# Performance work log

Hardware: AMD Instinct MI355X
Metric: run time of the kernel (lower is better)

## Reference

```python
import jax, jax.numpy as jnp
import numpy as np

SEQ, BATCH, N_IN, N_HID, N_OUT = 2048, 64, 256, 512, 128


def setup_inputs() -> dict:
    key = jax.random.key(0)
    ks = jax.random.split(key, 7)
    s_ih = 1.0 / np.sqrt(N_IN)
    s_hh = 1.0 / np.sqrt(N_HID)
    return {
        "x": jax.random.normal(ks[0], (SEQ, BATCH, N_IN), dtype=jnp.float32),
        # PyTorch Linear stores weight as (out_features, in_features)
        "W_ih": jax.random.uniform(ks[1], (N_HID, N_IN), jnp.float32, -s_ih, s_ih),
        "b_ih": jax.random.uniform(ks[2], (N_HID,), jnp.float32, -s_ih, s_ih),
        "W_hh": jax.random.uniform(ks[3], (N_HID, N_HID), jnp.float32, -s_hh, s_hh),
        "b_hh": jax.random.uniform(ks[4], (N_HID,), jnp.float32, -s_hh, s_hh),
        "W_ho": jax.random.uniform(ks[5], (N_OUT, N_HID), jnp.float32, -s_hh, s_hh),
        "b_ho": jax.random.uniform(ks[6], (N_OUT,), jnp.float32, -s_hh, s_hh),
    }


def reference(x, W_ih, b_ih, W_hh, b_hh, W_ho, b_ho):
    # hidden init: torch.zeros(1, n_hidden) broadcasts to (batch, n_hidden)
    h0 = jnp.zeros((x.shape[1], W_hh.shape[0]), dtype=x.dtype)

    def step(h, xt):
        # new_h = tanh(Linear_ih(x_t) + Linear_hh(h))
        h_new = jnp.tanh(xt @ W_ih.T + b_ih + h @ W_hh.T + b_hh)
        return h_new, None

    h_final, _ = jax.lax.scan(step, h0, x)
    return h_final @ W_ho.T + b_ho  # (batch, n_output)
```

## Files before the change

kernel.cpp:

```cpp
#include <hip/hip_runtime.h>
#include <math.h>

#define SEQ   2048
#define BATCH 64
#define NIN   256
#define NHID  512
#define NOUT  128

#define NSL 4
#define JSL 128

#define WIRE_WORDS (2*BATCH*NSL*256)
#define WIRE_BYTES ((size_t)WIRE_WORDS*4)
#define HFIN_BYTES ((size_t)BATCH*NHID*4)
#define XP_BYTES   ((size_t)SEQ*BATCH*NHID*4)

typedef unsigned int u32;
typedef u32 u32x2 __attribute__((ext_vector_type(2)));

__device__ __forceinline__ u32x2 ld8_ic(const u32* p) {
  u32x2 r;
  asm volatile("global_load_dwordx2 %0, %1, off sc0 sc1"
               : "=v"(r) : "v"(p) : "memory");
  return r;
}
__device__ __forceinline__ void st8_ic(u32* p, u32x2 v) {
  asm volatile("global_store_dwordx2 %0, %1, off sc0 sc1"
               :: "v"(p), "v"(v) : "memory");
}
__device__ __forceinline__ void wait_vm0() {
  asm volatile("s_waitcnt vmcnt(0)" ::: "memory");
  __builtin_amdgcn_sched_barrier(0);
}
__device__ __forceinline__ void pin4(float4& v) {
  asm volatile("" : "+v"(v.x), "+v"(v.y), "+v"(v.z), "+v"(v.w));
}

__device__ __forceinline__ float fast_tanh(float x) {
  const float e = __builtin_amdgcn_exp2f(x * 2.8853900817779268f);
  const float r = __builtin_amdgcn_rcpf(e + 1.0f);
  return fmaf(-2.0f, r, 1.0f);
}

__global__ __launch_bounds__(512, 1)
void xproj_kernel(const float* __restrict__ x,
                  const float* __restrict__ Wih,
                  const float* __restrict__ bih,
                  const float* __restrict__ bhh,
                  float* __restrict__ xp)
{
  const int bj = blockIdx.x & 7;
  const int bm = blockIdx.x >> 3;
  const int tid = threadIdx.x;
  const int tx = tid & 15, ty = tid >> 4;

  __shared__ __align__(16) float  wT[NIN][68];
  __shared__ __align__(16) float4 xS[64][66];

  for (int it = 0; it < 32; ++it) {
    const int widx = tid + (it << 9);
    const int k = widx >> 6, j = widx & 63;
    wT[k][j] = Wih[(size_t)(bj*64 + j)*NIN + k];
  }
  const int jg = bj*64 + tx*4;
  float4 bv;
  bv.x = bih[jg+0]+bhh[jg+0]; bv.y = bih[jg+1]+bhh[jg+1];
  bv.z = bih[jg+2]+bhh[jg+2]; bv.w = bih[jg+3]+bhh[jg+3];
  __syncthreads();

  for (int mt = 0; mt < 8; ++mt) {
    const size_t r0 = (size_t)bm*512 + mt*64;
    for (int it = 0; it < 8; ++it) {
      const int f = tid + (it << 9);
      const int m = f >> 6, kq = f & 63;
      xS[m][kq] = *(const float4*)&x[(r0 + m)*NIN + (kq << 2)];
    }
    __syncthreads();

    float acc[2][4];
    #pragma unroll
    for (int q = 0; q < 2; ++q)
      #pragma unroll
      for (int jj = 0; jj < 4; ++jj) acc[q][jj] = 0.f;

    for (int kq = 0; kq < 64; ++kq) {
      const float4 xv0 = xS[ty*2+0][kq];
      const float4 xv1 = xS[ty*2+1][kq];
      #pragma unroll
      for (int i = 0; i < 4; ++i) {
        const float4 wv = *(const float4*)&wT[(kq<<2)+i][tx*4];
        const float xi0 = (i==0)?xv0.x:(i==1)?xv0.y:(i==2)?xv0.z:xv0.w;
        const float xi1 = (i==0)?xv1.x:(i==1)?xv1.y:(i==2)?xv1.z:xv1.w;
        acc[0][0]=fmaf(xi0,wv.x,acc[0][0]); acc[0][1]=fmaf(xi0,wv.y,acc[0][1]);
        acc[0][2]=fmaf(xi0,wv.z,acc[0][2]); acc[0][3]=fmaf(xi0,wv.w,acc[0][3]);
        acc[1][0]=fmaf(xi1,wv.x,acc[1][0]); acc[1][1]=fmaf(xi1,wv.y,acc[1][1]);
        acc[1][2]=fmaf(xi1,wv.z,acc[1][2]); acc[1][3]=fmaf(xi1,wv.w,acc[1][3]);
      }
    }
    float4 o0, o1;
    o0.x = acc[0][0]+bv.x; o0.y = acc[0][1]+bv.y;
    o0.z = acc[0][2]+bv.z; o0.w = acc[0][3]+bv.w;
    o1.x = acc[1][0]+bv.x; o1.y = acc[1][1]+bv.y;
    o1.z = acc[1][2]+bv.z; o1.w = acc[1][3]+bv.w;
    *(float4*)&xp[(r0 + ty*2 + 0)*NHID + jg] = o0;
    *(float4*)&xp[(r0 + ty*2 + 1)*NHID + jg] = o1;
    __syncthreads();
  }
}

__global__ __launch_bounds__(1024)
__attribute__((amdgpu_waves_per_eu(4, 4)))
void rnn_seq4_kernel(const float* __restrict__ xp,
                     const float* __restrict__ Whh,
                     u32* __restrict__ wire,
                     float* __restrict__ hfin)
{
  const int bid = blockIdx.x;
  const int sj  = bid >> 6;
  const int b   = bid & 63;
  const int tid = threadIdx.x;
  const int jg  = tid >> 5;
  const int kl  = tid & 31;
  const int w   = tid >> 6, lane = tid & 63;

  __shared__ __align__(16) float hS[2][32][36];
  for (int i = tid; i < 2*32*36; i += 1024) (&hS[0][0][0])[i] = 0.f;

  const int j0 = sj*JSL + jg*4;
  const int k0 = kl*16;
  float4 w0[4], w1[4], w2[4], w3[4];
  #pragma unroll
  for (int i = 0; i < 4; ++i) {
    w0[i] = *(const float4*)&Whh[(size_t)(j0+0)*NHID + k0 + 4*i];
    w1[i] = *(const float4*)&Whh[(size_t)(j0+1)*NHID + k0 + 4*i];
    w2[i] = *(const float4*)&Whh[(size_t)(j0+2)*NHID + k0 + 4*i];
    w3[i] = *(const float4*)&Whh[(size_t)(j0+3)*NHID + k0 + 4*i];
  }
  #pragma unroll
  for (int i = 0; i < 4; ++i) { pin4(w0[i]); pin4(w1[i]); pin4(w2[i]); pin4(w3[i]); }

  const int jl = jg*4 + (kl & 3);
  const float* xptr = xp + (size_t)b*NHID + sj*JSL + jl;
  float xpC = *xptr;
  xptr += BATCH*NHID;

  const int sp = (sj + 1 + (w >> 1)) & 3;
  const int sm = ((w & 1) << 6) + lane;
  const int skg = sp*JSL + sm;
  const int srow = skg >> 4, scol = skg & 15;
  const int okg = sj*JSL + jl;
  const int orow = okg >> 4, ocol = okg & 15;

  const float* dA0 = &hS[0][kl][0];
  const float* dA1 = &hS[1][kl][0];
  float* pL0 = &hS[0][orow][ocol];
  float* pL1 = &hS[1][orow][ocol];
  float* sd0 = &hS[0][srow][scol];
  float* sd1 = &hS[1][srow][scol];
  u32* wo0 = wire + ((((size_t)0*BATCH + b)*NSL + sj) << 8) + (jl << 1);
  u32* wo1 = wire + ((((size_t)1*BATCH + b)*NSL + sj) << 8) + (jl << 1);
  const u32* wf0 = wire + ((((size_t)0*BATCH + b)*NSL + sp) << 8) + (sm << 1);
  const u32* wf1 = wire + ((((size_t)1*BATCH + b)*NSL + sp) << 8) + (sm << 1);

  __syncthreads();

  float hlast = 0.f;

#define RSTEP(T, DA, PL, WO, WF, SD)                                          \
  {                                                                           \
    const bool last_ = (T) == SEQ - 1;                                        \
    float xpN = 0.f;                                                          \
    if (!last_) { xpN = *xptr; xptr += BATCH*NHID; }                          \
    float a0=0.f, a1=0.f, a2=0.f, a3=0.f;                                     \
    _Pragma("unroll")                                                         \
    for (int i = 0; i < 4; ++i) {                                             \
      const float4 hv = *(const float4*)((DA) + 4*i);                         \
      a0=fmaf(w0[i].x,hv.x,a0); a0=fmaf(w0[i].y,hv.y,a0);                     \
      a0=fmaf(w0[i].z,hv.z,a0); a0=fmaf(w0[i].w,hv.w,a0);                     \
      a1=fmaf(w1[i].x,hv.x,a1); a1=fmaf(w1[i].y,hv.y,a1);                     \
      a1=fmaf(w1[i].z,hv.z,a1); a1=fmaf(w1[i].w,hv.w,a1);                     \
      a2=fmaf(w2[i].x,hv.x,a2); a2=fmaf(w2[i].y,hv.y,a2);                     \
      a2=fmaf(w2[i].z,hv.z,a2); a2=fmaf(w2[i].w,hv.w,a2);                     \
      a3=fmaf(w3[i].x,hv.x,a3); a3=fmaf(w3[i].y,hv.y,a3);                     \
      a3=fmaf(w3[i].z,hv.z,a3); a3=fmaf(w3[i].w,hv.w,a3);                     \
    }                                                                         \
    float s_;                                                                 \
    {                                                                         \
      const float t0_ = __shfl_xor(a0,1,64), t1_ = __shfl_xor(a1,1,64);       \
      const float t2_ = __shfl_xor(a2,1,64), t3_ = __shfl_xor(a3,1,64);       \
      float b0_, b1_;                                                         \
      if (kl & 1) { b0_ = a1 + t1_; b1_ = a3 + t3_; }                         \
      else        { b0_ = a0 + t0_; b1_ = a2 + t2_; }                         \
      const float u0_ = __shfl_xor(b0_,2,64), u1_ = __shfl_xor(b1_,2,64);     \
      s_ = (kl & 2) ? (b1_ + u1_) : (b0_ + u0_);                              \
      s_ += __shfl_xor(s_, 4, 64);                                            \
      s_ += __shfl_xor(s_, 8, 64);                                            \
      s_ += __shfl_xor(s_, 16, 64);                                           \
    }                                                                         \
    const float hn_ = fast_tanh(s_ + xpC);                                    \
    if (!last_) {                                                             \
      const u32 tg_ = (u32)(T) + 1u;                                          \
      if (kl < 4) {                                                           \
        *(PL) = hn_;                                                          \
        const u32 bits_ = __float_as_uint(hn_);                               \
        u32x2 pv_;                                                            \
        pv_.x = (tg_<<16) | (bits_>>16);                                      \
        pv_.y = (tg_<<16) | (bits_ & 0xffffu);                                \
        st8_ic((WO), pv_);                                                    \
      }                                                                       \
      if (w < 6) {                                                            \
        u32x2 v_ = ld8_ic(WF); wait_vm0();                                    \
        int guard_ = 1 << 17;                                                 \
        while (!__all((v_.x>>16)==tg_ && (v_.y>>16)==tg_)) {                  \
          if (--guard_ == 0) break;         \
          v_ = ld8_ic(WF); wait_vm0();                                        \
        }                                                                     \
        *(SD) = __uint_as_float((v_.x<<16) | (v_.y & 0xffffu));               \
      }                                                                       \
      __syncthreads();                             \
      xpC = xpN;                                                              \
    }                                                                         \
    hlast = hn_;                                                              \
  }

  for (int t = 0; t < SEQ; t += 2) {
    RSTEP(t,     dA0, pL1, wo1, wf1, sd1);
    RSTEP(t + 1, dA1, pL0, wo0, wf0, sd0);
  }
#undef RSTEP

  if (kl < 4) hfin[(size_t)b*NHID + sj*JSL + jl] = hlast;
}

__global__ __launch_bounds__(512, 2)
void rnn_seq_fb_kernel(const float* __restrict__ xp,
                       const float* __restrict__ Whh,
                       float* __restrict__ hfin)
{
  const int b = blockIdx.x;
  const int j = threadIdx.x;
  __shared__ __align__(16) float hh[2][NHID];
  hh[0][j] = 0.f;
  const float* wrow = Whh + (size_t)j*NHID;
  const float* xcol = xp + (size_t)b*NHID + j;
  float xpC = xcol[0];
  float hnew = 0.f;
  __syncthreads();
  for (int t = 0; t < SEQ; ++t) {
    const int par = t & 1;
    float xpN = 0.f;
    if (t + 1 < SEQ) xpN = xcol[(size_t)(t+1)*(BATCH*NHID)];
    const float* hA = hh[par];
    float a0=0.f,a1=0.f,a2=0.f,a3=0.f;
    #pragma unroll 8
    for (int kq = 0; kq < 128; ++kq) {
      const float4 wv = *(const float4*)&wrow[kq << 2];
      const float4 hv = *(const float4*)&hA[kq << 2];
      a0 = fmaf(wv.x, hv.x, a0);
      a1 = fmaf(wv.y, hv.y, a1);
      a2 = fmaf(wv.z, hv.z, a2);
      a3 = fmaf(wv.w, hv.w, a3);
    }
    hnew = tanhf((a0+a1)+(a2+a3) + xpC);
    hh[par ^ 1][j] = hnew;
    xpC = xpN;
    __syncthreads();
  }
  hfin[(size_t)b*NHID + j] = hnew;
}

__global__ __launch_bounds__(NOUT, 1)
void rnn_out_kernel(const float* __restrict__ hfin,
                    const float* __restrict__ Who,
                    const float* __restrict__ bho,
                    float* __restrict__ out)
{
  const int b = blockIdx.x;
  const int o = threadIdx.x;
  __shared__ __align__(16) float hB[NHID];
  for (int k = o; k < NHID; k += NOUT) hB[k] = hfin[(size_t)b*NHID + k];
  __syncthreads();
  const float* wr = Who + (size_t)o*NHID;
  float a0=0.f,a1=0.f,a2=0.f,a3=0.f;
  for (int k = 0; k < NHID; k += 4) {
    const float4 wv = *(const float4*)&wr[k];
    a0 = fmaf(wv.x, hB[k  ], a0);
    a1 = fmaf(wv.y, hB[k+1], a1);
    a2 = fmaf(wv.z, hB[k+2], a2);
    a3 = fmaf(wv.w, hB[k+3], a3);
  }
  out[(size_t)b*NOUT + o] = (a0+a1)+(a2+a3) + bho[o];
}

extern "C" void kernel_launch(void* const* d_in, const int* in_sizes, int n_in,
                              void* d_out, int out_size, void* d_ws, size_t ws_size,
                              hipStream_t stream)
{
  const float* x   = (const float*)d_in[0];
  const float* Wih = (const float*)d_in[1];
  const float* bih = (const float*)d_in[2];
  const float* Whh = (const float*)d_in[3];
  const float* bhh = (const float*)d_in[4];
  const float* Who = (const float*)d_in[5];
  const float* bho = (const float*)d_in[6];
  float* out = (float*)d_out;

  const size_t need = WIRE_BYTES + HFIN_BYTES + XP_BYTES;

  if (ws_size >= need) {
    u32*   wire = (u32*)d_ws;
    float* hfin = (float*)((char*)d_ws + WIRE_BYTES);
    float* xp   = (float*)((char*)d_ws + WIRE_BYTES + HFIN_BYTES);

    hipMemsetAsync(wire, 0, WIRE_BYTES, stream);
    xproj_kernel  <<<dim3(2048), dim3(512), 0, stream>>>(x, Wih, bih, bhh, xp);
    rnn_seq4_kernel<<<dim3(NSL*BATCH), dim3(1024), 0, stream>>>(xp, Whh, wire, hfin);
    rnn_out_kernel<<<dim3(BATCH), dim3(NOUT), 0, stream>>>(hfin, Who, bho, out);
  } else {
    float* hfin = (float*)d_ws;
    float* xp   = (float*)((char*)d_ws + HFIN_BYTES);
    xproj_kernel<<<dim3(2048), dim3(512), 0, stream>>>(x, Wih, bih, bhh, xp);
    rnn_seq_fb_kernel<<<dim3(BATCH), dim3(512), 0, stream>>>(xp, Whh, hfin);
    rnn_out_kernel<<<dim3(BATCH), dim3(NOUT), 0, stream>>>(hfin, Who, bho, out);
  }
}
```

Baseline: 4.750 ms.

## Split hidden dim into 8 slices with two batch rows per block

Restructures the recurrent kernel so each 512-thread block owns a 64-wide slice of the hidden state for two batch rows, using 8 slices instead of 4 with 1024-thread blocks. Each weight element is reused across two batch rows and the reduction tree is widened to 8 accumulators. The W_hh fragment is now reloaded from global/cache every two steps instead of being pinned in registers, trading memory traffic for lower register pressure. The spin-wait now polls two wire slots per wave, and cross-block communication fans in from 7 peer slices.

```diff
diff --git a/kernel.cpp b/kernel.cpp
--- a/kernel.cpp
+++ b/kernel.cpp
@@ -7,10 +7,10 @@
 #define NHID  512
 #define NOUT  128
 
-#define NSL 4
-#define JSL 128
-
-#define WIRE_WORDS (2*BATCH*NSL*256)
+#define NSL 8
+#define JSL 64
+
+#define WIRE_WORDS (2*BATCH*NSL*128)
 #define WIRE_BYTES ((size_t)WIRE_WORDS*4)
 #define HFIN_BYTES ((size_t)BATCH*NHID*4)
 #define XP_BYTES   ((size_t)SEQ*BATCH*NHID*4)
@@ -31,9 +31,6 @@
 __device__ __forceinline__ void wait_vm0() {
   asm volatile("s_waitcnt vmcnt(0)" ::: "memory");
   __builtin_amdgcn_sched_barrier(0);
-}
-__device__ __forceinline__ void pin4(float4& v) {
-  asm volatile("" : "+v"(v.x), "+v"(v.y), "+v"(v.z), "+v"(v.w));
 }
 
 __device__ __forceinline__ float fast_tanh(float x) {
@@ -108,99 +105,109 @@
   }
 }
 
-__global__ __launch_bounds__(1024)
-__attribute__((amdgpu_waves_per_eu(4, 4)))
-void rnn_seq4_kernel(const float* __restrict__ xp,
+__global__ __launch_bounds__(512, 2)
+void rnn_seq8_kernel(const float* __restrict__ xp,
                      const float* __restrict__ Whh,
                      u32* __restrict__ wire,
                      float* __restrict__ hfin)
 {
   const int bid = blockIdx.x;
-  const int sj  = bid >> 6;
-  const int b   = bid & 63;
+  const int bp  = bid >> 3;
+  const int sj  = bid & 7;
   const int tid = threadIdx.x;
   const int jg  = tid >> 5;
   const int kl  = tid & 31;
   const int w   = tid >> 6, lane = tid & 63;
 
-  __shared__ __align__(16) float hS[2][32][36];
-  for (int i = tid; i < 2*32*36; i += 1024) (&hS[0][0][0])[i] = 0.f;
-
-  const int j0 = sj*JSL + jg*4;
-  const int k0 = kl*16;
-  float4 w0[4], w1[4], w2[4], w3[4];
-  #pragma unroll
-  for (int i = 0; i < 4; ++i) {
-    w0[i] = *(const float4*)&Whh[(size_t)(j0+0)*NHID + k0 + 4*i];
-    w1[i] = *(const float4*)&Whh[(size_t)(j0+1)*NHID + k0 + 4*i];
-    w2[i] = *(const float4*)&Whh[(size_t)(j0+2)*NHID + k0 + 4*i];
-    w3[i] = *(const float4*)&Whh[(size_t)(j0+3)*NHID + k0 + 4*i];
-  }
-  #pragma unroll
-  for (int i = 0; i < 4; ++i) { pin4(w0[i]); pin4(w1[i]); pin4(w2[i]); pin4(w3[i]); }
-
-  const int jl = jg*4 + (kl & 3);
-  const float* xptr = xp + (size_t)b*NHID + sj*JSL + jl;
+  __shared__ __align__(16) float hS[2][2][32][36];
+  for (int i = tid; i < 2*2*32*36; i += 512) (&hS[0][0][0][0])[i] = 0.f;
+
+  const int jloc  = jg*4 + ((kl >> 1) & 3);
+  const int rr    = kl & 1;
+  const int bown  = bp*2 + rr;
+  const int jglob = sj*JSL + jloc;
+
+  const float* xptr = xp + (size_t)bown*NHID + jglob;
   float xpC = *xptr;
   xptr += BATCH*NHID;
 
-  const int sp = (sj + 1 + (w >> 1)) & 3;
-  const int sm = ((w & 1) << 6) + lane;
-  const int skg = sp*JSL + sm;
-  const int srow = skg >> 4, scol = skg & 15;
-  const int okg = sj*JSL + jl;
-  const int orow = okg >> 4, ocol = okg & 15;
-
-  const float* dA0 = &hS[0][kl][0];
-  const float* dA1 = &hS[1][kl][0];
-  float* pL0 = &hS[0][orow][ocol];
-  float* pL1 = &hS[1][orow][ocol];
-  float* sd0 = &hS[0][srow][scol];
-  float* sd1 = &hS[1][srow][scol];
-  u32* wo0 = wire + ((((size_t)0*BATCH + b)*NSL + sj) << 8) + (jl << 1);
-  u32* wo1 = wire + ((((size_t)1*BATCH + b)*NSL + sj) << 8) + (jl << 1);
-  const u32* wf0 = wire + ((((size_t)0*BATCH + b)*NSL + sp) << 8) + (sm << 1);
-  const u32* wf1 = wire + ((((size_t)1*BATCH + b)*NSL + sp) << 8) + (sm << 1);
+  const float* wb = Whh + (size_t)(sj*JSL + jg*4)*NHID + kl*16;
+
+  u32* wo0 = wire + ((((size_t)0*BATCH + bown)*NSL + sj) << 7) + (jloc << 1);
+  u32* wo1 = wire + ((((size_t)1*BATCH + bown)*NSL + sj) << 7) + (jloc << 1);
+  const int okc = sj*4 + (jloc >> 4), okk = jloc & 15;
+  float* pL0 = &hS[0][rr][okc][okk];
+  float* pL1 = &hS[1][rr][okc][okk];
+
+  const int sp = (sj + 1 + w) & 7;
+  const u32* wfa0 = wire + ((((size_t)0*BATCH + bp*2+0)*NSL + sp) << 7) + (lane << 1);
+  const u32* wfa1 = wire + ((((size_t)0*BATCH + bp*2+1)*NSL + sp) << 7) + (lane << 1);
+  const u32* wfb0 = wire + ((((size_t)1*BATCH + bp*2+0)*NSL + sp) << 7) + (lane << 1);
+  const u32* wfb1 = wire + ((((size_t)1*BATCH + bp*2+1)*NSL + sp) << 7) + (lane << 1);
+  const int skc = sp*4 + (lane >> 4), skk = lane & 15;
+  float* sda0 = &hS[0][0][skc][skk];
+  float* sda1 = &hS[0][1][skc][skk];
+  float* sdb0 = &hS[1][0][skc][skk];
+  float* sdb1 = &hS[1][1][skc][skk];
+
+  const float* dA0 = &hS[0][0][kl][0];
+  const float* dA1 = &hS[1][0][kl][0];
+  const int DROW = 32*36;
 
   __syncthreads();
-
   float hlast = 0.f;
 
-#define RSTEP(T, DA, PL, WO, WF, SD)                                          \
+#define RSTEP(T, DA, PL, WO, WF0, WF1, SD0, SD1)                              \
   {                                                                           \
     const bool last_ = (T) == SEQ - 1;                                        \
     float xpN = 0.f;                                                          \
     if (!last_) { xpN = *xptr; xptr += BATCH*NHID; }                          \
-    float a0=0.f, a1=0.f, a2=0.f, a3=0.f;                                     \
+    float A0=0.f,A1=0.f,A2=0.f,A3=0.f,A4=0.f,A5=0.f,A6=0.f,A7=0.f;            \
     _Pragma("unroll")                                                         \
     for (int i = 0; i < 4; ++i) {                                             \
-      const float4 hv = *(const float4*)((DA) + 4*i);                         \
-      a0=fmaf(w0[i].x,hv.x,a0); a0=fmaf(w0[i].y,hv.y,a0);                     \
-      a0=fmaf(w0[i].z,hv.z,a0); a0=fmaf(w0[i].w,hv.w,a0);                     \
-      a1=fmaf(w1[i].x,hv.x,a1); a1=fmaf(w1[i].y,hv.y,a1);                     \
-      a1=fmaf(w1[i].z,hv.z,a1); a1=fmaf(w1[i].w,hv.w,a1);                     \
-      a2=fmaf(w2[i].x,hv.x,a2); a2=fmaf(w2[i].y,hv.y,a2);                     \
-      a2=fmaf(w2[i].z,hv.z,a2); a2=fmaf(w2[i].w,hv.w,a2);                     \
-      a3=fmaf(w3[i].x,hv.x,a3); a3=fmaf(w3[i].y,hv.y,a3);                     \
-      a3=fmaf(w3[i].z,hv.z,a3); a3=fmaf(w3[i].w,hv.w,a3);                     \
+      const float4 h0 = *(const float4*)((DA) + 4*i);                         \
+      const float4 h1 = *(const float4*)((DA) + DROW + 4*i);                  \
+      A0=fmaf(w0[i].x,h0.x,A0); A0=fmaf(w0[i].y,h0.y,A0);                     \
+      A0=fmaf(w0[i].z,h0.z,A0); A0=fmaf(w0[i].w,h0.w,A0);                     \
+      A1=fmaf(w0[i].x,h1.x,A1); A1=fmaf(w0[i].y,h1.y,A1);                     \
+      A1=fmaf(w0[i].z,h1.z,A1); A1=fmaf(w0[i].w,h1.w,A1);                     \
+      A2=fmaf(w1[i].x,h0.x,A2); A2=fmaf(w1[i].y,h0.y,A2);                     \
+      A2=fmaf(w1[i].z,h0.z,A2); A2=fmaf(w1[i].w,h0.w,A2);                     \
+      A3=fmaf(w1[i].x,h1.x,A3); A3=fmaf(w1[i].y,h1.y,A3);                     \
+      A3=fmaf(w1[i].z,h1.z,A3); A3=fmaf(w1[i].w,h1.w,A3);                     \
+      A4=fmaf(w2[i].x,h0.x,A4); A4=fmaf(w2[i].y,h0.y,A4);                     \
+      A4=fmaf(w2[i].z,h0.z,A4); A4=fmaf(w2[i].w,h0.w,A4);                     \
+      A5=fmaf(w2[i].x,h1.x,A5); A5=fmaf(w2[i].y,h1.y,A5);                     \
+      A5=fmaf(w2[i].z,h1.z,A5); A5=fmaf(w2[i].w,h1.w,A5);                     \
+      A6=fmaf(w3[i].x,h0.x,A6); A6=fmaf(w3[i].y,h0.y,A6);                     \
+      A6=fmaf(w3[i].z,h0.z,A6); A6=fmaf(w3[i].w,h0.w,A6);                     \
+      A7=fmaf(w3[i].x,h1.x,A7); A7=fmaf(w3[i].y,h1.y,A7);                     \
+      A7=fmaf(w3[i].z,h1.z,A7); A7=fmaf(w3[i].w,h1.w,A7);                     \
     }                                                                         \
+      \
     float s_;                                                                 \
     {                                                                         \
-      const float t0_ = __shfl_xor(a0,1,64), t1_ = __shfl_xor(a1,1,64);       \
-      const float t2_ = __shfl_xor(a2,1,64), t3_ = __shfl_xor(a3,1,64);       \
-      float b0_, b1_;                                                         \
-      if (kl & 1) { b0_ = a1 + t1_; b1_ = a3 + t3_; }                         \
-      else        { b0_ = a0 + t0_; b1_ = a2 + t2_; }                         \
-      const float u0_ = __shfl_xor(b0_,2,64), u1_ = __shfl_xor(b1_,2,64);     \
-      s_ = (kl & 2) ? (b1_ + u1_) : (b0_ + u0_);                              \
-      s_ += __shfl_xor(s_, 4, 64);                                            \
-      s_ += __shfl_xor(s_, 8, 64);                                            \
-      s_ += __shfl_xor(s_, 16, 64);                                           \
+      const float t0_=__shfl_xor(A0,1,32), t1_=__shfl_xor(A1,1,32);           \
+      const float t2_=__shfl_xor(A2,1,32), t3_=__shfl_xor(A3,1,32);           \
+      const float t4_=__shfl_xor(A4,1,32), t5_=__shfl_xor(A5,1,32);           \
+      const float t6_=__shfl_xor(A6,1,32), t7_=__shfl_xor(A7,1,32);           \
+      float B0_,B1_,B2_,B3_;                                                  \
+      if (kl & 1) { B0_=A1+t1_; B1_=A3+t3_; B2_=A5+t5_; B3_=A7+t7_; }         \
+      else        { B0_=A0+t0_; B1_=A2+t2_; B2_=A4+t4_; B3_=A6+t6_; }         \
+      const float u0_=__shfl_xor(B0_,2,32), u1_=__shfl_xor(B1_,2,32);         \
+      const float u2_=__shfl_xor(B2_,2,32), u3_=__shfl_xor(B3_,2,32);         \
+      float C0_,C1_;                                                          \
+      if (kl & 2) { C0_=B1_+u1_; C1_=B3_+u3_; }                               \
+      else        { C0_=B0_+u0_; C1_=B2_+u2_; }                               \
+      const float v0_=__shfl_xor(C0_,4,32), v1_=__shfl_xor(C1_,4,32);         \
+      s_ = (kl & 4) ? (C1_+v1_) : (C0_+v0_);                                  \
+      s_ += __shfl_xor(s_, 8, 32);                                            \
+      s_ += __shfl_xor(s_, 16, 32);                                           \
     }                                                                         \
     const float hn_ = fast_tanh(s_ + xpC);                                    \
     if (!last_) {                                                             \
       const u32 tg_ = (u32)(T) + 1u;                                          \
-      if (kl < 4) {                                                           \
+      if (kl < 8) {                                                           \
         *(PL) = hn_;                                                          \
         const u32 bits_ = __float_as_uint(hn_);                               \
         u32x2 pv_;                                                            \
@@ -208,14 +215,26 @@
         pv_.y = (tg_<<16) | (bits_ & 0xffffu);                                \
         st8_ic((WO), pv_);                                                    \
       }                                                                       \
-      if (w < 6) {                                                            \
-        u32x2 v_ = ld8_ic(WF); wait_vm0();                                    \
-        int guard_ = 1 << 17;                                                 \
-        while (!__all((v_.x>>16)==tg_ && (v_.y>>16)==tg_)) {                  \
-          if (--guard_ == 0) break;         \
-          v_ = ld8_ic(WF); wait_vm0();                                        \
+      if (w < 7) {                                                            \
+        u32x2 va_ = ld8_ic(WF0), vb_ = ld8_ic(WF1);                           \
+        wait_vm0();                                                           \
+        u32 pend_ = 3u; int g_ = 1 << 17;                                     \
+        for (;;) {                                                            \
+          const bool ok0_ = __all((va_.x>>16)==tg_ && (va_.y>>16)==tg_);      \
+          const bool ok1_ = __all((vb_.x>>16)==tg_ && (vb_.y>>16)==tg_);      \
+          if ((pend_&1u) && ok0_) {                                           \
+            *(SD0) = __uint_as_float((va_.x<<16)|(va_.y&0xffffu));            \
+            pend_ &= ~1u;                                                     \
+          }                                                                   \
+          if ((pend_&2u) && ok1_) {                                           \
+            *(SD1) = __uint_as_float((vb_.x<<16)|(vb_.y&0xffffu));            \
+            pend_ &= ~2u;                                                     \
+          }                                                                   \
+          if (!pend_ || --g_ == 0) break;   \
+          if (pend_&1u) va_ = ld8_ic(WF0);                                    \
+          if (pend_&2u) vb_ = ld8_ic(WF1);                                    \
+          wait_vm0();                                                         \
         }                                                                     \
-        *(SD) = __uint_as_float((v_.x<<16) | (v_.y & 0xffffu));               \
       }                                                                       \
       __syncthreads();                             \
       xpC = xpN;                                                              \
@@ -224,12 +243,22 @@
   }
 
   for (int t = 0; t < SEQ; t += 2) {
-    RSTEP(t,     dA0, pL1, wo1, wf1, sd1);
-    RSTEP(t + 1, dA1, pL0, wo0, wf0, sd0);
+    const float* wp = wb;
+    asm volatile("" : "+v"(wp));
+    float4 w0[4], w1[4], w2[4], w3[4];
+    #pragma unroll
+    for (int i = 0; i < 4; ++i) {
+      w0[i] = *(const float4*)(wp + 0*NHID + 4*i);
+      w1[i] = *(const float4*)(wp + 1*NHID + 4*i);
+      w2[i] = *(const float4*)(wp + 2*NHID + 4*i);
+      w3[i] = *(const float4*)(wp + 3*NHID + 4*i);
+    }
+    RSTEP(t,     dA0, pL1, wo1, wfb0, wfb1, sdb0, sdb1);
+    RSTEP(t + 1, dA1, pL0, wo0, wfa0, wfa1, sda0, sda1);
   }
 #undef RSTEP
 
-  if (kl < 4) hfin[(size_t)b*NHID + sj*JSL + jl] = hlast;
+  if (kl < 8) hfin[(size_t)bown*NHID + jglob] = hlast;
 }
 
 __global__ __launch_bounds__(512, 2)
@@ -313,8 +342,8 @@
     float* xp   = (float*)((char*)d_ws + WIRE_BYTES + HFIN_BYTES);
 
     hipMemsetAsync(wire, 0, WIRE_BYTES, stream);
-    xproj_kernel  <<<dim3(2048), dim3(512), 0, stream>>>(x, Wih, bih, bhh, xp);
-    rnn_seq4_kernel<<<dim3(NSL*BATCH), dim3(1024), 0, stream>>>(xp, Whh, wire, hfin);
+    xproj_kernel <<<dim3(2048), dim3(512), 0, stream>>>(x, Wih, bih, bhh, xp);
+    rnn_seq8_kernel<<<dim3(256), dim3(512), 0, stream>>>(xp, Whh, wire, hfin);
     rnn_out_kernel<<<dim3(BATCH), dim3(NOUT), 0, stream>>>(hfin, Who, bho, out);
   } else {
     float* hfin = (float*)d_ws;
```

Result: slower. 6.865 ms (+44.5%).
